# Optimization experiments

Hardware: AMD Instinct MI355X
Metric: run time of the kernel (lower is better)

## Reference

```python
import jax, jax.numpy as jnp
import numpy as np

D, H1, O, E = 1024, 4096, 1024, 8
B = 8192


def setup_inputs() -> dict:
    key = jax.random.key(0)
    k1, k2, k3, k4 = jax.random.split(key, 4)
    # kaiming_uniform_ with nonlinearity='relu': bound = sqrt(6 / fan_in), fan_in = last dim
    b_w1 = float(np.sqrt(6.0 / D))
    b_w2 = float(np.sqrt(6.0 / H1))
    x = jax.random.normal(k1, (B, D), dtype=jnp.float32)
    eid = jax.random.randint(k2, (B,), 0, E, dtype=jnp.int32)
    W1 = jax.random.uniform(k3, (E, H1, D), dtype=jnp.float32, minval=-b_w1, maxval=b_w1)
    W2 = jax.random.uniform(k4, (E, O, H1), dtype=jnp.float32, minval=-b_w2, maxval=b_w2)
    b2 = jnp.zeros((E, O), dtype=jnp.float32)
    return {"x": x, "eid": eid, "W1": W1, "W2": W2, "b2": b2}


def reference(x, eid, W1, W2, b2):
    # Per-token expert MLP: y_i = gelu(x_i @ W1[eid_i].T) @ W2[eid_i].T + b2[eid_i]
    # Dense-dispatch formulation: loop over the (small, static) expert axis,
    # compute each expert MLP on all tokens, and select per-token via mask.
    # Math is identical to the sort/gather/scatter original.
    y = jnp.zeros((x.shape[0], W2.shape[1]), dtype=x.dtype)
    for e in range(W1.shape[0]):
        h = jax.nn.gelu(x @ W1[e].T, approximate=False)   # [B, H1]
        y_e = h @ W2[e].T + b2[e]                          # [B, O]
        mask = (eid == e)[:, None].astype(x.dtype)
        y = y + mask * y_e
    return y
```

## Files before the change

### kernel.cpp

```cpp
#include <hip/hip_runtime.h>
#include <hip/hip_bf16.h>
#include <math.h>

constexpr int kD  = 1024;
constexpr int kH1 = 4096;
constexpr int kO  = 1024;
constexpr int kE  = 8;
constexpr int kB  = 8192;

constexpr int BM   = 128;
constexpr int MAXT = kB / BM + kE;

typedef __attribute__((ext_vector_type(8))) short short8;
typedef __attribute__((ext_vector_type(4))) float f32x4;

__device__ __forceinline__ unsigned short f2bf(float f) {
  unsigned int u = __float_as_uint(f);
  u += 0x7fffu + ((u >> 16) & 1u);
  return (unsigned short)(u >> 16);
}

__device__ __forceinline__ float gelu_fast(float x) {
  float u = 0.7978845608028654f * (x + 0.044715f * x * x * x);
  float eu = __expf(2.0f * u);
  float th = 1.0f - 2.0f / (eu + 1.0f);
  return 0.5f * x * (1.0f + th);
}

__global__ __launch_bounds__(256) void setup_kernel(const int* __restrict__ eid,
                                                    int* __restrict__ perm,
                                                    int* __restrict__ tiles) {
  __shared__ int cnt[kE];
  __shared__ int off[kE];
  __shared__ int cur[kE];
  int t = threadIdx.x;
  if (t < kE) { cnt[t] = 0; cur[t] = 0; }
  __syncthreads();
  for (int i = t; i < kB; i += 256) atomicAdd(&cnt[eid[i]], 1);
  __syncthreads();
  if (t == 0) {
    int o = 0, nt = 0;
    for (int e = 0; e < kE; ++e) {
      off[e] = o;
      int c = cnt[e];
      for (int r = 0; r < c; r += BM) {
        tiles[nt * 4 + 0] = e;
        tiles[nt * 4 + 1] = o + r;
        tiles[nt * 4 + 2] = (c - r < BM) ? (c - r) : BM;
        tiles[nt * 4 + 3] = 0;
        ++nt;
      }
      o += c;
    }
    for (; nt < MAXT; ++nt) {
      tiles[nt * 4 + 0] = 0; tiles[nt * 4 + 1] = 0;
      tiles[nt * 4 + 2] = 0; tiles[nt * 4 + 3] = 0;
    }
  }
  __syncthreads();
  for (int i = t; i < kB; i += 256) {
    int e = eid[i];
    int p = off[e] + atomicAdd(&cur[e], 1);
    perm[p] = i;
  }
}

__global__ __launch_bounds__(256) void gather_kernel(const float* __restrict__ x,
                                                     const int* __restrict__ perm,
                                                     unsigned short* __restrict__ xg) {
  int idx = blockIdx.x * 256 + threadIdx.x;
  int pos = idx >> 7;
  int c   = (idx & 127) << 3;
  int row = perm[pos];
  const float4* s = (const float4*)(x + (size_t)row * kD + c);
  float4 f0 = s[0], f1 = s[1];
  short8 v;
  v[0] = (short)f2bf(f0.x); v[1] = (short)f2bf(f0.y);
  v[2] = (short)f2bf(f0.z); v[3] = (short)f2bf(f0.w);
  v[4] = (short)f2bf(f1.x); v[5] = (short)f2bf(f1.y);
  v[6] = (short)f2bf(f1.z); v[7] = (short)f2bf(f1.w);
  *(short8*)(xg + (size_t)pos * kD + c) = v;
}

constexpr int kCN  = kE * kH1 * kD / 8;

__global__ __launch_bounds__(256) void convert_kernel(const float* __restrict__ src,
                                                      unsigned short* __restrict__ dst,
                                                      int n8) {
  int stride = gridDim.x * 256;
  for (int i = blockIdx.x * 256 + threadIdx.x; i < n8; i += stride) {
    const float4* s = (const float4*)(src + (size_t)i * 8);
    float4 f0 = s[0], f1 = s[1];
    short8 v;
    v[0] = (short)f2bf(f0.x); v[1] = (short)f2bf(f0.y);
    v[2] = (short)f2bf(f0.z); v[3] = (short)f2bf(f0.w);
    v[4] = (short)f2bf(f1.x); v[5] = (short)f2bf(f1.y);
    v[6] = (short)f2bf(f1.z); v[7] = (short)f2bf(f1.w);
    *(short8*)(dst + (size_t)i * 8) = v;
  }
}

template <int KTOT, int N, int NPAN, int MODE>
__global__ __launch_bounds__(512, 2) void gemm32_kernel(
    const unsigned short* __restrict__ Amat,
    const unsigned short* __restrict__ Bmat,
    const float* __restrict__ bias,
    const int* __restrict__ tiles,
    const int* __restrict__ perm,
    unsigned short* __restrict__ out_bf,
    float* __restrict__ out_f) {
  extern __shared__ char lds[];
  constexpr int NKt = KTOT / 32;
  constexpr int TOTAL = MAXT * NPAN;
  constexpr int cpx = TOTAL / 8;
  constexpr int nchN = (NPAN >= 4) ? NPAN / 4 : 1;

  const int bid = blockIdx.x;
  const int id = (bid & 7) * cpx + (bid >> 3);
  const int chunk = id >> 4, a16 = id & 15;
  const int ti = (chunk / nchN) * 4 + (a16 & 3);
  const int n0 = ((chunk % nchN) * 4 + (a16 >> 2)) * 256;

  const int e  = tiles[ti * 4 + 0];
  const int rs = tiles[ti * 4 + 1];
  const int nr = tiles[ti * 4 + 2];
  if (nr == 0) return;

  const int t = threadIdx.x;
  const int l = t & 63;
  const int w = t >> 6;
  const int lr = l & 15, g = l >> 4;
  const int wr = w >> 2;
  const int wc = w & 3;

  const unsigned short* Bp = Bmat + (size_t)e * N * KTOT;

  const int sR = t >> 2;
  const int sG = (t & 3) ^ ((sR >> 1) & 3);
  const unsigned short* ArowS = Amat + (size_t)(rs + sR) * KTOT + sG * 8;
  const unsigned short* BrowS0 = Bp + (size_t)(n0 + sR) * KTOT + sG * 8;
  const unsigned short* BrowS1 = Bp + (size_t)(n0 + 128 + sR) * KTOT + sG * 8;

  auto stageA = [&](char* buf, int k0) {
    __builtin_amdgcn_global_load_lds(
        (const __attribute__((address_space(1))) unsigned int*)(ArowS + k0),
        (__attribute__((address_space(3))) unsigned int*)(buf + t * 16), 16, 0, 0);
  };
  auto stageB = [&](char* buf, int k0, int i) {
    const unsigned short* src = (i ? BrowS1 : BrowS0) + k0;
    __builtin_amdgcn_global_load_lds(
        (const __attribute__((address_space(1))) unsigned int*)src,
        (__attribute__((address_space(3))) unsigned int*)(buf + 8192 + i * 8192 + t * 16),
        16, 0, 0);
  };

  const int rA = wr * 64 + lr;
  const int rB = wc * 64 + lr;
  const int offA0 = rA * 64 + ((g ^ ((rA >> 1) & 3)) * 16);
  const int offB0 = 8192 + rB * 64 + ((g ^ ((rB >> 1) & 3)) * 16);

  short8 aF[4], bF[4];
  f32x4 acc[4][4] = {};

  auto readA = [&](char* buf) {
#pragma unroll
    for (int mr = 0; mr < 4; ++mr)
      aF[mr] = *(const short8*)(buf + offA0 + mr * 1024);
  };
  auto readB2 = [&](char* buf, int nclo) {
#pragma unroll
    for (int j = 0; j < 2; ++j)
      bF[nclo + j] = *(const short8*)(buf + offB0 + (nclo + j) * 1024);
  };
  auto mfmaH = [&](int nclo) {
    __builtin_amdgcn_s_setprio(1);
#pragma unroll
    for (int j = 0; j < 2; ++j)
#pragma unroll
      for (int mr = 0; mr < 4; ++mr)
        acc[nclo + j][mr] = __builtin_amdgcn_mfma_f32_16x16x32_bf16(
            aF[mr], bF[nclo + j], acc[nclo + j][mr], 0, 0, 0);
    __builtin_amdgcn_s_setprio(0);
  };

  char* b0 = lds;
  char* b1 = lds + 24576;
  char* b2 = lds + 49152;

  stageA(b0, 0);  stageB(b0, 0, 0);  stageB(b0, 0, 1);
  stageA(b1, 32); stageB(b1, 32, 0); stageB(b1, 32, 1);

#pragma unroll 1
  for (int kt = 0; kt < NKt; ++kt) {
    const int k0n = (kt + 2) * 32;
    const bool more = (kt + 2 < NKt);
    if (kt == NKt - 1) asm volatile("s_waitcnt vmcnt(0)" ::: "memory");
    else               asm volatile("s_waitcnt vmcnt(3)" ::: "memory");
    __builtin_amdgcn_s_barrier();
    readA(b0);
    readB2(b0, 0);
    if (more) stageA(b2, k0n);
    __builtin_amdgcn_s_barrier();
    mfmaH(0);
    __builtin_amdgcn_s_barrier();
    readB2(b0, 2);
    if (more) { stageB(b2, k0n, 0); stageB(b2, k0n, 1); }
    __builtin_amdgcn_s_barrier();
    mfmaH(2);
    char* tmp = b0; b0 = b1; b1 = b2; b2 = tmp;
  }

  const int lr4 = g * 4;
#pragma unroll
  for (int mr = 0; mr < 4; ++mr)
#pragma unroll
    for (int rg = 0; rg < 4; ++rg) {
      int row = wr * 64 + mr * 16 + lr4 + rg;
      if (row < nr) {
        if constexpr (MODE == 0) {
          unsigned short* dst = out_bf + (size_t)(rs + row) * N + n0 + wc * 64;
#pragma unroll
          for (int nc = 0; nc < 4; ++nc)
            dst[nc * 16 + lr] = f2bf(gelu_fast(acc[nc][mr][rg]));
        } else {
          int orig = perm[rs + row];
          float* dst = out_f + (size_t)orig * N + n0 + wc * 64;
          const float* bp = bias + (size_t)e * N + n0 + wc * 64;
#pragma unroll
          for (int nc = 0; nc < 4; ++nc)
            dst[nc * 16 + lr] = acc[nc][mr][rg] + bp[nc * 16 + lr];
        }
      }
    }
}

extern "C" void kernel_launch(void* const* d_in, const int* in_sizes, int n_in,
                              void* d_out, int out_size, void* d_ws, size_t ws_size,
                              hipStream_t stream) {
  const float* x  = (const float*)d_in[0];
  const int*  eid = (const int*)d_in[1];
  const float* W1 = (const float*)d_in[2];
  const float* W2 = (const float*)d_in[3];
  const float* b2 = (const float*)d_in[4];
  float* y = (float*)d_out;

  char* ws = (char*)d_ws;
  int* perm  = (int*)ws;
  int* tiles = (int*)(ws + 32768);
  unsigned short* xg = (unsigned short*)(ws + 36864);
  size_t xg_bytes = (size_t)(kB + 128) * kD * 2;
  unsigned short* h  = (unsigned short*)(ws + 36864 + xg_bytes);
  size_t h_bytes = (size_t)(kB + 128) * kH1 * 2;
  size_t w1b_off = 36864 + xg_bytes + h_bytes;
  unsigned short* W1b = (unsigned short*)(ws + w1b_off);
  size_t w2b_off = w1b_off + 67108864;
  const bool twobuf = ws_size >= w2b_off + 67108864;
  unsigned short* W2b = twobuf ? (unsigned short*)(ws + w2b_off) : W1b;

  auto g1 = gemm32_kernel<kD, kH1, 16, 0>;
  auto g2 = gemm32_kernel<kH1, kO, 4, 1>;
  hipFuncSetAttribute((const void*)g1, hipFuncAttributeMaxDynamicSharedMemorySize, 73728);
  hipFuncSetAttribute((const void*)g2, hipFuncAttributeMaxDynamicSharedMemorySize, 73728);

  setup_kernel<<<1, 256, 0, stream>>>(eid, perm, tiles);
  gather_kernel<<<(kB * kD / 8) / 256, 256, 0, stream>>>(x, perm, xg);

  convert_kernel<<<2048, 256, 0, stream>>>(W1, W1b, kCN);
  g1<<<MAXT * 16, 512, 73728, stream>>>(xg, W1b, nullptr, tiles, perm, h, nullptr);

  convert_kernel<<<2048, 256, 0, stream>>>(W2, W2b, kCN);
  g2<<<MAXT * 4, 512, 73728, stream>>>(h, W2b, b2, tiles, perm, nullptr, y);
}
```

Measured before the change: 310.1 us.

## Fuse gather with W1 conversion and overlap W2 conversion with first GEMM

Merges the token gather/bf16 cast and the W1 fp32-to-bf16 conversion into one prep kernel launch. When the workspace has room for two weight buffers, the W2 conversion moves into extra leading blocks of the first GEMM launch, so it runs alongside the GEMM tiles instead of as a separate serialized kernel. This removes launch gaps and lets memory-bound conversion overlap compute-bound GEMM work, at the cost of the conversion blocks competing with GEMM blocks for bandwidth and CU slots.

```diff
diff --git a/kernel.cpp b/kernel.cpp
--- a/kernel.cpp
+++ b/kernel.cpp
@@ -25,6 +25,18 @@
   float eu = __expf(2.0f * u);
   float th = 1.0f - 2.0f / (eu + 1.0f);
   return 0.5f * x * (1.0f + th);
+}
+
+__device__ __forceinline__ void cvt8(const float* __restrict__ src,
+                                     unsigned short* __restrict__ dst) {
+  const float4* s = (const float4*)src;
+  float4 f0 = s[0], f1 = s[1];
+  short8 v;
+  v[0] = (short)f2bf(f0.x); v[1] = (short)f2bf(f0.y);
+  v[2] = (short)f2bf(f0.z); v[3] = (short)f2bf(f0.w);
+  v[4] = (short)f2bf(f1.x); v[5] = (short)f2bf(f1.y);
+  v[6] = (short)f2bf(f1.z); v[7] = (short)f2bf(f1.w);
+  *(short8*)dst = v;
 }
 
 __global__ __launch_bounds__(256) void setup_kernel(const int* __restrict__ eid,
@@ -65,42 +77,36 @@
   }
 }
 
-__global__ __launch_bounds__(256) void gather_kernel(const float* __restrict__ x,
-                                                     const int* __restrict__ perm,
-                                                     unsigned short* __restrict__ xg) {
-  int idx = blockIdx.x * 256 + threadIdx.x;
-  int pos = idx >> 7;
-  int c   = (idx & 127) << 3;
-  int row = perm[pos];
-  const float4* s = (const float4*)(x + (size_t)row * kD + c);
-  float4 f0 = s[0], f1 = s[1];
-  short8 v;
-  v[0] = (short)f2bf(f0.x); v[1] = (short)f2bf(f0.y);
-  v[2] = (short)f2bf(f0.z); v[3] = (short)f2bf(f0.w);
-  v[4] = (short)f2bf(f1.x); v[5] = (short)f2bf(f1.y);
-  v[6] = (short)f2bf(f1.z); v[7] = (short)f2bf(f1.w);
-  *(short8*)(xg + (size_t)pos * kD + c) = v;
-}
-
-constexpr int kCN  = kE * kH1 * kD / 8;
+constexpr int kGB = kB * kD / 8 / 256;
+constexpr int kCN = kE * kH1 * kD / 8;
+
+__global__ __launch_bounds__(256) void prep_kernel(
+    const float* __restrict__ x, const int* __restrict__ perm,
+    unsigned short* __restrict__ xg,
+    const float* __restrict__ W1, unsigned short* __restrict__ W1b) {
+  const int b = blockIdx.x;
+  if (b < kGB) {
+    int idx = b * 256 + threadIdx.x;
+    int pos = idx >> 7;
+    int c   = (idx & 127) << 3;
+    cvt8(x + (size_t)perm[pos] * kD + c, xg + (size_t)pos * kD + c);
+  } else {
+    const int cb = b - kGB;
+    const int stride = 2048 * 256;
+    for (int i = cb * 256 + threadIdx.x; i < kCN; i += stride)
+      cvt8(W1 + (size_t)i * 8, W1b + (size_t)i * 8);
+  }
+}
 
 __global__ __launch_bounds__(256) void convert_kernel(const float* __restrict__ src,
                                                       unsigned short* __restrict__ dst,
                                                       int n8) {
   int stride = gridDim.x * 256;
-  for (int i = blockIdx.x * 256 + threadIdx.x; i < n8; i += stride) {
-    const float4* s = (const float4*)(src + (size_t)i * 8);
-    float4 f0 = s[0], f1 = s[1];
-    short8 v;
-    v[0] = (short)f2bf(f0.x); v[1] = (short)f2bf(f0.y);
-    v[2] = (short)f2bf(f0.z); v[3] = (short)f2bf(f0.w);
-    v[4] = (short)f2bf(f1.x); v[5] = (short)f2bf(f1.y);
-    v[6] = (short)f2bf(f1.z); v[7] = (short)f2bf(f1.w);
-    *(short8*)(dst + (size_t)i * 8) = v;
-  }
-}
-
-template <int KTOT, int N, int NPAN, int MODE>
+  for (int i = blockIdx.x * 256 + threadIdx.x; i < n8; i += stride)
+    cvt8(src + (size_t)i * 8, dst + (size_t)i * 8);
+}
+
+template <int KTOT, int N, int NPAN, int MODE, int CONVW2>
 __global__ __launch_bounds__(512, 2) void gemm32_kernel(
     const unsigned short* __restrict__ Amat,
     const unsigned short* __restrict__ Bmat,
@@ -108,14 +114,29 @@
     const int* __restrict__ tiles,
     const int* __restrict__ perm,
     unsigned short* __restrict__ out_bf,
-    float* __restrict__ out_f) {
+    float* __restrict__ out_f,
+    const float* __restrict__ csrc,
+    unsigned short* __restrict__ cdst) {
   extern __shared__ char lds[];
   constexpr int NKt = KTOT / 32;
   constexpr int TOTAL = MAXT * NPAN;
   constexpr int cpx = TOTAL / 8;
   constexpr int nchN = (NPAN >= 4) ? NPAN / 4 : 1;
 
-  const int bid = blockIdx.x;
+  int bid = blockIdx.x;
+  const int t = threadIdx.x;
+
+  if constexpr (CONVW2 > 0) {
+    if (bid < 256) {
+      constexpr int per = kCN / 256;
+      size_t u0 = (size_t)bid * per;
+      for (int i = t; i < per; i += 512)
+        cvt8(csrc + (u0 + i) * 8, cdst + (u0 + i) * 8);
+      return;
+    }
+    bid -= 256;
+  }
+
   const int id = (bid & 7) * cpx + (bid >> 3);
   const int chunk = id >> 4, a16 = id & 15;
   const int ti = (chunk / nchN) * 4 + (a16 & 3);
@@ -126,7 +147,6 @@
   const int nr = tiles[ti * 4 + 2];
   if (nr == 0) return;
 
-  const int t = threadIdx.x;
   const int l = t & 63;
   const int w = t >> 6;
   const int lr = l & 15, g = l >> 4;
@@ -257,17 +277,26 @@
   const bool twobuf = ws_size >= w2b_off + 67108864;
   unsigned short* W2b = twobuf ? (unsigned short*)(ws + w2b_off) : W1b;
 
-  auto g1 = gemm32_kernel<kD, kH1, 16, 0>;
-  auto g2 = gemm32_kernel<kH1, kO, 4, 1>;
-  hipFuncSetAttribute((const void*)g1, hipFuncAttributeMaxDynamicSharedMemorySize, 73728);
-  hipFuncSetAttribute((const void*)g2, hipFuncAttributeMaxDynamicSharedMemorySize, 73728);
+  auto g1f = gemm32_kernel<kD, kH1, 16, 0, 1>;
+  auto g1s = gemm32_kernel<kD, kH1, 16, 0, 0>;
+  auto g2  = gemm32_kernel<kH1, kO, 4, 1, 0>;
+  hipFuncSetAttribute((const void*)g1f, hipFuncAttributeMaxDynamicSharedMemorySize, 73728);
+  hipFuncSetAttribute((const void*)g1s, hipFuncAttributeMaxDynamicSharedMemorySize, 73728);
+  hipFuncSetAttribute((const void*)g2,  hipFuncAttributeMaxDynamicSharedMemorySize, 73728);
 
   setup_kernel<<<1, 256, 0, stream>>>(eid, perm, tiles);
-  gather_kernel<<<(kB * kD / 8) / 256, 256, 0, stream>>>(x, perm, xg);
-
-  convert_kernel<<<2048, 256, 0, stream>>>(W1, W1b, kCN);
-  g1<<<MAXT * 16, 512, 73728, stream>>>(xg, W1b, nullptr, tiles, perm, h, nullptr);
-
-  convert_kernel<<<2048, 256, 0, stream>>>(W2, W2b, kCN);
-  g2<<<MAXT * 4, 512, 73728, stream>>>(h, W2b, b2, tiles, perm, nullptr, y);
-}
+
+  prep_kernel<<<kGB + 2048, 256, 0, stream>>>(x, perm, xg, W1, W1b);
+
+  if (twobuf) {
+    g1f<<<256 + MAXT * 16, 512, 73728, stream>>>(
+        xg, W1b, nullptr, tiles, perm, h, nullptr, W2, W2b);
+  } else {
+    g1s<<<MAXT * 16, 512, 73728, stream>>>(
+        xg, W1b, nullptr, tiles, perm, h, nullptr, nullptr, nullptr);
+    convert_kernel<<<2048, 256, 0, stream>>>(W2, W2b, kCN);
+  }
+
+  g2<<<MAXT * 4, 512, 73728, stream>>>(
+      h, W2b, b2, tiles, perm, nullptr, y, nullptr, nullptr);
+}
```

Measured after the change: 303.2 us. 2.2% less time.

## Fuse fp32-to-bf16 weight conversion into GEMM B-operand staging

Applied to the files above, without the earlier changes.

Drops the separate weight conversion kernels and has each GEMM stage fp32 weight tiles straight into LDS, converting them to bf16 in registers just before the MFMAs. The pipeline goes from three LDS buffers to two, and the B tile doubles in size because it stays fp32. This removes a full read and write of both 64 MB weight tensors, but each weight tile is now re-read in fp32 by every row tile, which doubles the L2/HBM traffic on the B side. It also adds conversion ALU work inside the main loop, and a launch-bounds hint of 4 blocks per SM cannot be met with 80 KB of LDS per block.

```diff
diff --git a/kernel.cpp b/kernel.cpp
--- a/kernel.cpp
+++ b/kernel.cpp
@@ -18,6 +18,11 @@
   unsigned int u = __float_as_uint(f);
   u += 0x7fffu + ((u >> 16) & 1u);
   return (unsigned short)(u >> 16);
+}
+
+__device__ __forceinline__ unsigned int pk2(float a, float b) {
+  __hip_bfloat162 h = __float22bfloat162_rn(make_float2(a, b));
+  return *reinterpret_cast<unsigned int*>(&h);
 }
 
 __device__ __forceinline__ float gelu_fast(float x) {
@@ -82,28 +87,10 @@
   *(short8*)(xg + (size_t)pos * kD + c) = v;
 }
 
-constexpr int kCN  = kE * kH1 * kD / 8;
-
-__global__ __launch_bounds__(256) void convert_kernel(const float* __restrict__ src,
-                                                      unsigned short* __restrict__ dst,
-                                                      int n8) {
-  int stride = gridDim.x * 256;
-  for (int i = blockIdx.x * 256 + threadIdx.x; i < n8; i += stride) {
-    const float4* s = (const float4*)(src + (size_t)i * 8);
-    float4 f0 = s[0], f1 = s[1];
-    short8 v;
-    v[0] = (short)f2bf(f0.x); v[1] = (short)f2bf(f0.y);
-    v[2] = (short)f2bf(f0.z); v[3] = (short)f2bf(f0.w);
-    v[4] = (short)f2bf(f1.x); v[5] = (short)f2bf(f1.y);
-    v[6] = (short)f2bf(f1.z); v[7] = (short)f2bf(f1.w);
-    *(short8*)(dst + (size_t)i * 8) = v;
-  }
-}
-
 template <int KTOT, int N, int NPAN, int MODE>
-__global__ __launch_bounds__(512, 2) void gemm32_kernel(
+__global__ __launch_bounds__(512, 4) void gemmfd_kernel(
     const unsigned short* __restrict__ Amat,
-    const unsigned short* __restrict__ Bmat,
+    const float* __restrict__ Wmat,
     const float* __restrict__ bias,
     const int* __restrict__ tiles,
     const int* __restrict__ perm,
@@ -133,33 +120,37 @@
   const int wr = w >> 2;
   const int wc = w & 3;
 
-  const unsigned short* Bp = Bmat + (size_t)e * N * KTOT;
+  const float* Bp = Wmat + ((size_t)e * N + n0) * KTOT;
 
   const int sR = t >> 2;
   const int sG = (t & 3) ^ ((sR >> 1) & 3);
   const unsigned short* ArowS = Amat + (size_t)(rs + sR) * KTOT + sG * 8;
-  const unsigned short* BrowS0 = Bp + (size_t)(n0 + sR) * KTOT + sG * 8;
-  const unsigned short* BrowS1 = Bp + (size_t)(n0 + 128 + sR) * KTOT + sG * 8;
 
   auto stageA = [&](char* buf, int k0) {
     __builtin_amdgcn_global_load_lds(
         (const __attribute__((address_space(1))) unsigned int*)(ArowS + k0),
         (__attribute__((address_space(3))) unsigned int*)(buf + t * 16), 16, 0, 0);
   };
+
+  const int sRB = t >> 3;
+  const int sGB = (t & 7) ^ (sRB & 7);
+  const float* BrowS = Bp + (size_t)sRB * KTOT + sGB * 4;
   auto stageB = [&](char* buf, int k0, int i) {
-    const unsigned short* src = (i ? BrowS1 : BrowS0) + k0;
+    const float* src = BrowS + (size_t)i * 64 * KTOT + k0;
     __builtin_amdgcn_global_load_lds(
         (const __attribute__((address_space(1))) unsigned int*)src,
-        (__attribute__((address_space(3))) unsigned int*)(buf + 8192 + i * 8192 + t * 16),
+        (__attribute__((address_space(3))) unsigned int*)(buf + 8192 + (i * 512 + t) * 16),
         16, 0, 0);
   };
 
   const int rA = wr * 64 + lr;
-  const int rB = wc * 64 + lr;
   const int offA0 = rA * 64 + ((g ^ ((rA >> 1) & 3)) * 16);
-  const int offB0 = 8192 + rB * 64 + ((g ^ ((rB >> 1) & 3)) * 16);
-
-  short8 aF[4], bF[4];
+  const int rB0 = wc * 64 + lr;
+  const int offB_h0 = 8192 + rB0 * 128 + (((2 * g + 0) ^ (lr & 7)) * 16);
+  const int offB_h1 = 8192 + rB0 * 128 + (((2 * g + 1) ^ (lr & 7)) * 16);
+
+  short8 aF[4], bFh[2];
+  float4 Bff[2][2];
   f32x4 acc[4][4] = {};
 
   auto readA = [&](char* buf) {
@@ -167,10 +158,23 @@
     for (int mr = 0; mr < 4; ++mr)
       aF[mr] = *(const short8*)(buf + offA0 + mr * 1024);
   };
-  auto readB2 = [&](char* buf, int nclo) {
-#pragma unroll
-    for (int j = 0; j < 2; ++j)
-      bF[nclo + j] = *(const short8*)(buf + offB0 + (nclo + j) * 1024);
+  auto readBf = [&](char* buf, int half) {
+#pragma unroll
+    for (int j = 0; j < 2; ++j) {
+      Bff[j][0] = *(const float4*)(buf + offB_h0 + (half * 2 + j) * 2048);
+      Bff[j][1] = *(const float4*)(buf + offB_h1 + (half * 2 + j) * 2048);
+    }
+  };
+  auto cvtB = [&]() {
+#pragma unroll
+    for (int j = 0; j < 2; ++j) {
+      union { unsigned int u[4]; short8 v; } un;
+      un.u[0] = pk2(Bff[j][0].x, Bff[j][0].y);
+      un.u[1] = pk2(Bff[j][0].z, Bff[j][0].w);
+      un.u[2] = pk2(Bff[j][1].x, Bff[j][1].y);
+      un.u[3] = pk2(Bff[j][1].z, Bff[j][1].w);
+      bFh[j] = un.v;
+    }
   };
   auto mfmaH = [&](int nclo) {
     __builtin_amdgcn_s_setprio(1);
@@ -179,35 +183,38 @@
 #pragma unroll
       for (int mr = 0; mr < 4; ++mr)
         acc[nclo + j][mr] = __builtin_amdgcn_mfma_f32_16x16x32_bf16(
-            aF[mr], bF[nclo + j], acc[nclo + j][mr], 0, 0, 0);
+            aF[mr], bFh[j], acc[nclo + j][mr], 0, 0, 0);
     __builtin_amdgcn_s_setprio(0);
   };
 
-  char* b0 = lds;
-  char* b1 = lds + 24576;
-  char* b2 = lds + 49152;
-
-  stageA(b0, 0);  stageB(b0, 0, 0);  stageB(b0, 0, 1);
-  stageA(b1, 32); stageB(b1, 32, 0); stageB(b1, 32, 1);
+  stageA(lds, 0);
+  stageB(lds, 0, 0); stageB(lds, 0, 1);
+  stageB(lds, 0, 2); stageB(lds, 0, 3);
 
 #pragma unroll 1
   for (int kt = 0; kt < NKt; ++kt) {
-    const int k0n = (kt + 2) * 32;
-    const bool more = (kt + 2 < NKt);
-    if (kt == NKt - 1) asm volatile("s_waitcnt vmcnt(0)" ::: "memory");
-    else               asm volatile("s_waitcnt vmcnt(3)" ::: "memory");
-    __builtin_amdgcn_s_barrier();
-    readA(b0);
-    readB2(b0, 0);
-    if (more) stageA(b2, k0n);
-    __builtin_amdgcn_s_barrier();
+    char* cur = lds + (size_t)((kt & 1) * 40960);
+    char* oth = lds + (size_t)(((kt & 1) ^ 1) * 40960);
+    const bool more = (kt + 1 < NKt);
+    const int k0n = (kt + 1) * 32;
+    if (more) {
+      stageA(oth, k0n); stageB(oth, k0n, 0); stageB(oth, k0n, 1);
+      asm volatile("s_waitcnt vmcnt(3)" ::: "memory");
+    } else {
+      asm volatile("s_waitcnt vmcnt(0)" ::: "memory");
+    }
+    __builtin_amdgcn_s_barrier();
+    readA(cur);
+    readBf(cur, 0);
+    __builtin_amdgcn_s_barrier();
+    cvtB();
     mfmaH(0);
     __builtin_amdgcn_s_barrier();
-    readB2(b0, 2);
-    if (more) { stageB(b2, k0n, 0); stageB(b2, k0n, 1); }
-    __builtin_amdgcn_s_barrier();
+    readBf(cur, 1);
+    if (more) { stageB(oth, k0n, 2); stageB(oth, k0n, 3); }
+    __builtin_amdgcn_s_barrier();
+    cvtB();
     mfmaH(2);
-    char* tmp = b0; b0 = b1; b1 = b2; b2 = tmp;
   }
 
   const int lr4 = g * 4;
@@ -250,24 +257,16 @@
   unsigned short* xg = (unsigned short*)(ws + 36864);
   size_t xg_bytes = (size_t)(kB + 128) * kD * 2;
   unsigned short* h  = (unsigned short*)(ws + 36864 + xg_bytes);
-  size_t h_bytes = (size_t)(kB + 128) * kH1 * 2;
-  size_t w1b_off = 36864 + xg_bytes + h_bytes;
-  unsigned short* W1b = (unsigned short*)(ws + w1b_off);
-  size_t w2b_off = w1b_off + 67108864;
-  const bool twobuf = ws_size >= w2b_off + 67108864;
-  unsigned short* W2b = twobuf ? (unsigned short*)(ws + w2b_off) : W1b;
-
-  auto g1 = gemm32_kernel<kD, kH1, 16, 0>;
-  auto g2 = gemm32_kernel<kH1, kO, 4, 1>;
-  hipFuncSetAttribute((const void*)g1, hipFuncAttributeMaxDynamicSharedMemorySize, 73728);
-  hipFuncSetAttribute((const void*)g2, hipFuncAttributeMaxDynamicSharedMemorySize, 73728);
+
+  auto g1 = gemmfd_kernel<kD, kH1, 16, 0>;
+  auto g2 = gemmfd_kernel<kH1, kO, 4, 1>;
+  (void)hipFuncSetAttribute((const void*)g1, hipFuncAttributeMaxDynamicSharedMemorySize, 81920);
+  (void)hipFuncSetAttribute((const void*)g2, hipFuncAttributeMaxDynamicSharedMemorySize, 81920);
 
   setup_kernel<<<1, 256, 0, stream>>>(eid, perm, tiles);
   gather_kernel<<<(kB * kD / 8) / 256, 256, 0, stream>>>(x, perm, xg);
 
-  convert_kernel<<<2048, 256, 0, stream>>>(W1, W1b, kCN);
-  g1<<<MAXT * 16, 512, 73728, stream>>>(xg, W1b, nullptr, tiles, perm, h, nullptr);
-
-  convert_kernel<<<2048, 256, 0, stream>>>(W2, W2b, kCN);
-  g2<<<MAXT * 4, 512, 73728, stream>>>(h, W2b, b2, tiles, perm, nullptr, y);
-}
+  g1<<<MAXT * 16, 512, 81920, stream>>>(xg, W1, nullptr, tiles, perm, h, nullptr);
+
+  g2<<<MAXT * 4, 512, 81920, stream>>>(h, W2, b2, tiles, perm, nullptr, y);
+}
```

After: 391.6 us. 26.3% more time.
